# Kernel tuning notes

Measured on AMD Instinct MI355X. Metric: run time of the kernel, lower is better.

The kernel has to match this reference:

```python
import jax, jax.numpy as jnp
import numpy as np

B, LMAX, NCOND, NHID = 256, 512, 300, 600

def setup_inputs() -> dict:
    key = jax.random.key(0)
    ks = jax.random.split(key, 7)
    x = jax.random.normal(ks[0], (B, NCOND), dtype=jnp.float32)
    context = jax.random.normal(ks[1], (B, LMAX, NCOND), dtype=jnp.float32)
    lengths = jax.random.randint(ks[2], (B,), 0, LMAX, dtype=jnp.int32)
    W1 = jax.random.normal(ks[3], (NCOND, NHID), dtype=jnp.float32) * (1.0 / np.sqrt(NCOND))
    b1 = jax.random.normal(ks[4], (NHID,), dtype=jnp.float32) * 0.02
    Wa = jax.random.normal(ks[5], (NHID, NCOND), dtype=jnp.float32) * (1.0 / np.sqrt(NHID))
    ba = jax.random.normal(ks[6], (NCOND,), dtype=jnp.float32) * 0.02
    return {"x": x, "context": context, "lengths": lengths, "W1": W1, "b1": b1, "Wa": Wa, "ba": ba}

def reference(x, context, lengths, W1, b1, Wa, ba):
    # lengths clamped to >=1 (a ragged context is always non-empty)
    lens = jnp.maximum(lengths, 1)
    # valid-position mask over padded context: [B, L, 1]
    valid = (jnp.arange(LMAX)[None, :] < lens[:, None])[..., None].astype(context.dtype)
    # per-token MLP: relu(ctx @ W1 + b1)  -> [B, L, nhid]
    h = jax.nn.relu(jnp.einsum('blc,ch->blh', context, W1) + b1)
    # masked mean over valid tokens (ragged mean-pool) -> [B, nhid]
    pooled = jnp.sum(h * valid, axis=1) / lens[:, None].astype(context.dtype)
    # sigmoid gate -> [B, ncond], applied to x embeddings
    gate = jax.nn.sigmoid(jnp.einsum('bh,hc->bc', pooled, Wa) + ba)
    return gate * x
```

## Files before the change

### kernel.cpp

```cpp
#include <hip/hip_runtime.h>
#include <math.h>

#define BB     256
#define LMAX   512
#define NCOND  300
#define NHID   600
#define NSEG   8
#define CHUNK  64
#define KPAD   320
#define KLDS   328
#define NKC    10

#define AS1 __attribute__((address_space(1)))
#define AS3 __attribute__((address_space(3)))

typedef short s16x8 __attribute__((ext_vector_type(8)));
typedef float f32x4 __attribute__((ext_vector_type(4)));
typedef unsigned short u16x4 __attribute__((ext_vector_type(4)));

__device__ inline unsigned short f2bf(float f) {
    unsigned int x = __float_as_uint(f);
    x += 0x7fffu + ((x >> 16) & 1u);
    return (unsigned short)(x >> 16);
}

__global__ __launch_bounds__(256) void k0_w1t(const float* __restrict__ W1,
                                              unsigned short* __restrict__ w1t)
{
    const int t     = blockIdx.x * 256 + threadIdx.x;
    const int lane  = t & 63;
    const int g     = t >> 6;
    const int ntile = g / NKC;
    const int kc    = g - ntile * NKC;
    const int n     = ntile * 16 + (lane & 15);
    const int kbase = kc * 32 + (lane >> 4) * 8;
    union { unsigned short us[8]; s16x8 v8; } u;
#pragma unroll
    for (int j = 0; j < 8; ++j) {
        const int k = kbase + j;
        const float w = (n < NHID && k < NCOND) ? W1[(size_t)k * NHID + n] : 0.f;
        u.us[j] = f2bf(w);
    }
    *(s16x8*)(w1t + (size_t)t * 8) = u.v8;
}

__global__ __launch_bounds__(256) void k0b_cvt(const float* __restrict__ ctx,
                                               const int* __restrict__ lengths,
                                               unsigned short* __restrict__ ctx16)
{
    const int b = blockIdx.x, s = blockIdx.y, tid = threadIdx.x;
    int count = lengths[b]; if (count < 1) count = 1;
    if (s * CHUNK >= count) return;

    const size_t inbase  = ((size_t)b * LMAX + s * CHUNK) * NCOND;
    const float* src = ctx + inbase;
    char* dst = (char*)(ctx16 + ((size_t)b * LMAX + s * CHUNK) * KPAD);

#pragma unroll
    for (int i = 0; i < 20; ++i) {
        const int c   = i * 256 + tid;
        const int row = c / 80;
        const int q   = c - row * 80;
        float4 v = make_float4(0.f, 0.f, 0.f, 0.f);
        if (q < 75)
            v = *(const float4*)(src + (size_t)row * NCOND + q * 4);
        union { unsigned short us[4]; u16x4 v4; } o;
        o.us[0] = f2bf(v.x); o.us[1] = f2bf(v.y);
        o.us[2] = f2bf(v.z); o.us[3] = f2bf(v.w);
        const int off = (row * 640 + q * 8) ^ ((row & 7) << 4);
        *(u16x4*)(dst + off) = o.v4;
    }
}

__global__ __launch_bounds__(256, 3) void k1_mfma_dma(
    const unsigned short* __restrict__ ctx16, const int* __restrict__ lengths,
    const unsigned short* __restrict__ w1t, const float* __restrict__ b1,
    float* __restrict__ partial)
{
    const int b  = blockIdx.x;
    const int s  = blockIdx.y;
    const int ch = blockIdx.z;

    int count = lengths[b]; if (count < 1) count = 1;
    const int l0 = s * CHUNK;
    if (l0 >= count) return;
    const int valid = min(count - l0, CHUNK);

    const int tid  = threadIdx.x;
    const int lane = tid & 63;
    const int wv   = tid >> 6;
    const int ln15 = lane & 15;
    const int kg   = lane >> 4;

    __shared__ __align__(16) unsigned short atile[CHUNK * KPAD];

    const char* gsrc = (const char*)(ctx16 + ((size_t)b * LMAX + l0) * KPAD);
    char* lbase = (char*)atile;
#pragma unroll
    for (int r = 0; r < 10; ++r) {
        const int off = (r * 4 + wv) * 1024;
        __builtin_amdgcn_global_load_lds(
            (const AS1 void*)(gsrc + off + lane * 16),
            (AS3 void*)(lbase + off),
            16, 0, 0);
    }

    const int ntile0 = ch * 20 + wv * 5;
    const unsigned short* bbase = w1t + ((size_t)ntile0 * NKC * 64 + lane) * 8;
    s16x8 bf[2][5];
#pragma unroll
    for (int nt = 0; nt < 5; ++nt) bf[0][nt] = *(const s16x8*)(bbase + nt * 5120);

    __syncthreads();

    const int swz   = (ln15 & 7) << 4;
    const int abase = ln15 * 640 + kg * 16;
    const char* ab  = (const char*)atile;

    f32x4 acc[5][4];
#pragma unroll
    for (int nt = 0; nt < 5; ++nt)
#pragma unroll
        for (int mt = 0; mt < 4; ++mt) acc[nt][mt] = (f32x4){0.f, 0.f, 0.f, 0.f};

#pragma unroll
    for (int kc = 0; kc < NKC; ++kc) {
        const int cur = kc & 1, nxt = cur ^ 1;
        if (kc < NKC - 1) {
#pragma unroll
            for (int nt = 0; nt < 5; ++nt)
                bf[nxt][nt] = *(const s16x8*)(bbase + nt * 5120 + (kc + 1) * 512);
        }
        s16x8 af[4];
#pragma unroll
        for (int mt = 0; mt < 4; ++mt)
            af[mt] = *(const s16x8*)(ab + ((abase + mt * 10240 + kc * 64) ^ swz));
#pragma unroll
        for (int nt = 0; nt < 5; ++nt)
#pragma unroll
            for (int mt = 0; mt < 4; ++mt)
                acc[nt][mt] = __builtin_amdgcn_mfma_f32_16x16x32_bf16(
                    af[mt], bf[cur][nt], acc[nt][mt], 0, 0, 0);
    }

#pragma unroll
    for (int nt = 0; nt < 5; ++nt) {
        const int colg = ch * 320 + wv * 80 + nt * 16 + ln15;
        const float b1c = (colg < NHID) ? b1[colg] : 0.f;
        float ssum = 0.f;
#pragma unroll
        for (int mt = 0; mt < 4; ++mt) {
            const int rbase = mt * 16 + kg * 4;
#pragma unroll
            for (int r = 0; r < 4; ++r) {
                const float h = fmaxf(acc[nt][mt][r] + b1c, 0.f);
                if (rbase + r < valid) ssum += h;
            }
        }
        ssum += __shfl_xor(ssum, 16, 64);
        ssum += __shfl_xor(ssum, 32, 64);
        if (kg == 0 && colg < NHID)
            partial[((size_t)s * BB + b) * NHID + colg] = ssum;
    }
}

__global__ __launch_bounds__(256, 3) void k1_mfma_pool(
    const float* __restrict__ ctx, const int* __restrict__ lengths,
    const unsigned short* __restrict__ w1t, const float* __restrict__ b1,
    float* __restrict__ partial)
{
    const int b  = blockIdx.x;
    const int s  = blockIdx.y;
    const int ch = blockIdx.z;

    int count = lengths[b]; if (count < 1) count = 1;
    const int l0 = s * CHUNK;
    if (l0 >= count) return;
    const int valid = min(count - l0, CHUNK);

    const int tid  = threadIdx.x;
    const int lane = tid & 63;
    const int wv   = tid >> 6;
    const int ln15 = lane & 15;
    const int kg   = lane >> 4;

    __shared__ __align__(16) unsigned short atile[CHUNK * KLDS];

#pragma unroll
    for (int p = 0; p < 10; ++p) {
        const int i  = p * 256 + tid;
        const int r  = i / 40;
        const int c8 = i - r * 40;
        union { unsigned short us[8]; s16x8 v8; } u;
        if (r < valid && c8 < 38) {
            const float* src = ctx + ((size_t)b * LMAX + l0 + r) * NCOND + c8 * 8;
            const float4 v0 = *(const float4*)src;
            float4 v1 = make_float4(0.f, 0.f, 0.f, 0.f);
            if (c8 < 37) v1 = *(const float4*)(src + 4);
            u.us[0] = f2bf(v0.x); u.us[1] = f2bf(v0.y);
            u.us[2] = f2bf(v0.z); u.us[3] = f2bf(v0.w);
            u.us[4] = f2bf(v1.x); u.us[5] = f2bf(v1.y);
            u.us[6] = f2bf(v1.z); u.us[7] = f2bf(v1.w);
        } else {
#pragma unroll
            for (int j = 0; j < 8; ++j) u.us[j] = 0;
        }
        *(s16x8*)(atile + r * KLDS + c8 * 8) = u.v8;
    }
    __syncthreads();

    const int ntile0 = ch * 20 + wv * 5;
    const unsigned short* bbase = w1t + ((size_t)ntile0 * NKC * 64 + lane) * 8;
    const unsigned short* arow  = atile + ln15 * KLDS + kg * 8;

    f32x4 acc[5][4];
#pragma unroll
    for (int nt = 0; nt < 5; ++nt)
#pragma unroll
        for (int mt = 0; mt < 4; ++mt) acc[nt][mt] = (f32x4){0.f, 0.f, 0.f, 0.f};

    s16x8 bf[2][5];
#pragma unroll
    for (int nt = 0; nt < 5; ++nt) bf[0][nt] = *(const s16x8*)(bbase + nt * 5120);

#pragma unroll
    for (int kc = 0; kc < NKC; ++kc) {
        const int cur = kc & 1, nxt = cur ^ 1;
        if (kc < NKC - 1) {
#pragma unroll
            for (int nt = 0; nt < 5; ++nt)
                bf[nxt][nt] = *(const s16x8*)(bbase + nt * 5120 + (kc + 1) * 512);
        }
        s16x8 af[4];
#pragma unroll
        for (int mt = 0; mt < 4; ++mt)
            af[mt] = *(const s16x8*)(arow + mt * 16 * KLDS + kc * 32);
#pragma unroll
        for (int nt = 0; nt < 5; ++nt)
#pragma unroll
            for (int mt = 0; mt < 4; ++mt)
                acc[nt][mt] = __builtin_amdgcn_mfma_f32_16x16x32_bf16(
                    af[mt], bf[cur][nt], acc[nt][mt], 0, 0, 0);
    }

#pragma unroll
    for (int nt = 0; nt < 5; ++nt) {
        const int colg = ch * 320 + wv * 80 + nt * 16 + ln15;
        const float b1c = (colg < NHID) ? b1[colg] : 0.f;
        float ssum = 0.f;
#pragma unroll
        for (int mt = 0; mt < 4; ++mt) {
            const int rbase = mt * 16 + kg * 4;
#pragma unroll
            for (int r = 0; r < 4; ++r) {
                const float h = fmaxf(acc[nt][mt][r] + b1c, 0.f);
                if (rbase + r < valid) ssum += h;
            }
        }
        ssum += __shfl_xor(ssum, 16, 64);
        ssum += __shfl_xor(ssum, 32, 64);
        if (kg == 0 && colg < NHID)
            partial[((size_t)s * BB + b) * NHID + colg] = ssum;
    }
}

__global__ __launch_bounds__(640) void k2_gate(
    const float* __restrict__ x, const int* __restrict__ lengths,
    const float* __restrict__ partial, const float* __restrict__ Wa,
    const float* __restrict__ ba, float* __restrict__ out)
{
    const int b0  = blockIdx.x * 2;
    const int tid = threadIdx.x;

    __shared__ float pl[2][NHID];

    if (tid < NHID) {
#pragma unroll
        for (int bb = 0; bb < 2; ++bb) {
            int count = lengths[b0 + bb]; if (count < 1) count = 1;
            const int nch = (count + CHUNK - 1) >> 6;
            float ssum = 0.f;
            for (int sp = 0; sp < nch; ++sp)
                ssum += partial[((size_t)sp * BB + (b0 + bb)) * NHID + tid];
            pl[bb][tid] = ssum / (float)count;
        }
    }
    __syncthreads();

    if (tid < 2 * NCOND) {
        const int bb = tid / NCOND;
        const int n  = tid - bb * NCOND;
        const int b  = b0 + bb;
        float a0 = ba[n], a1 = 0.f, a2 = 0.f, a3 = 0.f;
        const float4* p4 = (const float4*)pl[bb];
        for (int h4 = 0; h4 < 148; h4 += 4) {
            const float4 pv0 = p4[h4];
            const float4 pv1 = p4[h4 + 1];
            const float4 pv2 = p4[h4 + 2];
            const float4 pv3 = p4[h4 + 3];
            const int hb = h4 * 4;
            a0 = fmaf(pv0.x, Wa[(size_t)(hb +  0) * NCOND + n], a0);
            a0 = fmaf(pv0.y, Wa[(size_t)(hb +  1) * NCOND + n], a0);
            a0 = fmaf(pv0.z, Wa[(size_t)(hb +  2) * NCOND + n], a0);
            a0 = fmaf(pv0.w, Wa[(size_t)(hb +  3) * NCOND + n], a0);
            a1 = fmaf(pv1.x, Wa[(size_t)(hb +  4) * NCOND + n], a1);
            a1 = fmaf(pv1.y, Wa[(size_t)(hb +  5) * NCOND + n], a1);
            a1 = fmaf(pv1.z, Wa[(size_t)(hb +  6) * NCOND + n], a1);
            a1 = fmaf(pv1.w, Wa[(size_t)(hb +  7) * NCOND + n], a1);
            a2 = fmaf(pv2.x, Wa[(size_t)(hb +  8) * NCOND + n], a2);
            a2 = fmaf(pv2.y, Wa[(size_t)(hb +  9) * NCOND + n], a2);
            a2 = fmaf(pv2.z, Wa[(size_t)(hb + 10) * NCOND + n], a2);
            a2 = fmaf(pv2.w, Wa[(size_t)(hb + 11) * NCOND + n], a2);
            a3 = fmaf(pv3.x, Wa[(size_t)(hb + 12) * NCOND + n], a3);
            a3 = fmaf(pv3.y, Wa[(size_t)(hb + 13) * NCOND + n], a3);
            a3 = fmaf(pv3.z, Wa[(size_t)(hb + 14) * NCOND + n], a3);
            a3 = fmaf(pv3.w, Wa[(size_t)(hb + 15) * NCOND + n], a3);
        }
        {
            const float4 pv0 = p4[148];
            const float4 pv1 = p4[149];
            a0 = fmaf(pv0.x, Wa[(size_t)592 * NCOND + n], a0);
            a0 = fmaf(pv0.y, Wa[(size_t)593 * NCOND + n], a0);
            a0 = fmaf(pv0.z, Wa[(size_t)594 * NCOND + n], a0);
            a0 = fmaf(pv0.w, Wa[(size_t)595 * NCOND + n], a0);
            a1 = fmaf(pv1.x, Wa[(size_t)596 * NCOND + n], a1);
            a1 = fmaf(pv1.y, Wa[(size_t)597 * NCOND + n], a1);
            a1 = fmaf(pv1.z, Wa[(size_t)598 * NCOND + n], a1);
            a1 = fmaf(pv1.w, Wa[(size_t)599 * NCOND + n], a1);
        }
        const float acc  = (a0 + a1) + (a2 + a3);
        const float gate = 1.0f / (1.0f + expf(-acc));
        out[(size_t)b * NCOND + n] = gate * x[(size_t)b * NCOND + n];
    }
}

extern "C" void kernel_launch(void* const* d_in, const int* in_sizes, int n_in,
                              void* d_out, int out_size, void* d_ws, size_t ws_size,
                              hipStream_t stream)
{
    const float* x       = (const float*)d_in[0];
    const float* ctx     = (const float*)d_in[1];
    const int*   lengths = (const int*)  d_in[2];
    const float* W1      = (const float*)d_in[3];
    const float* b1      = (const float*)d_in[4];
    const float* Wa      = (const float*)d_in[5];
    const float* ba      = (const float*)d_in[6];
    float*       out     = (float*)d_out;

    const size_t W1T_B   = 409600;
    const size_t PART_B  = 4915200;
    const size_t CTX16_B = (size_t)BB * LMAX * KPAD * 2;
    const size_t NEED    = W1T_B + PART_B + CTX16_B;

    unsigned short* w1t     = (unsigned short*)d_ws;
    float*          partial = (float*)((char*)d_ws + W1T_B);

    k0_w1t<<<100, 256, 0, stream>>>(W1, w1t);

    if (ws_size >= NEED) {
        unsigned short* ctx16 = (unsigned short*)((char*)d_ws + W1T_B + PART_B);
        k0b_cvt<<<dim3(BB, NSEG), 256, 0, stream>>>(ctx, lengths, ctx16);
        k1_mfma_dma<<<dim3(BB, NSEG, 2), 256, 0, stream>>>(ctx16, lengths, w1t, b1, partial);
    } else {
        k1_mfma_pool<<<dim3(BB, NSEG, 2), 256, 0, stream>>>(ctx, lengths, w1t, b1, partial);
    }

    k2_gate<<<BB / 2, 640, 0, stream>>>(x, lengths, partial, Wa, ba, out);
}
```

Measured before the change: 309.5 us.

## Split GEMM M dimension across 8 waves and widen bf16 conversion stores

The main MFMA kernel now uses 512 threads per block. Two wave halves each compute half of the 64 token rows, so each wave holds 10 accumulators instead of 20, and the halves' row sums are reduced through shared memory before the write. A-fragment LDS reads are double-buffered alongside the B loads. The conversion kernel now processes 8 floats per thread and issues 16-byte stores. The aim is more waves in flight and lower register pressure, at the cost of loading the B fragments twice per block and adding an extra barrier and reduction.

```diff
diff --git a/kernel.cpp b/kernel.cpp
--- a/kernel.cpp
+++ b/kernel.cpp
@@ -16,7 +16,7 @@
 
 typedef short s16x8 __attribute__((ext_vector_type(8)));
 typedef float f32x4 __attribute__((ext_vector_type(4)));
-typedef unsigned short u16x4 __attribute__((ext_vector_type(4)));
+typedef unsigned short u16x8 __attribute__((ext_vector_type(8)));
 
 __device__ inline unsigned short f2bf(float f) {
     unsigned int x = __float_as_uint(f);
@@ -52,27 +52,30 @@
     int count = lengths[b]; if (count < 1) count = 1;
     if (s * CHUNK >= count) return;
 
-    const size_t inbase  = ((size_t)b * LMAX + s * CHUNK) * NCOND;
-    const float* src = ctx + inbase;
+    const float* src = ctx + ((size_t)b * LMAX + s * CHUNK) * NCOND;
     char* dst = (char*)(ctx16 + ((size_t)b * LMAX + s * CHUNK) * KPAD);
 
 #pragma unroll
-    for (int i = 0; i < 20; ++i) {
+    for (int i = 0; i < 10; ++i) {
         const int c   = i * 256 + tid;
-        const int row = c / 80;
-        const int q   = c - row * 80;
-        float4 v = make_float4(0.f, 0.f, 0.f, 0.f);
-        if (q < 75)
-            v = *(const float4*)(src + (size_t)row * NCOND + q * 4);
-        union { unsigned short us[4]; u16x4 v4; } o;
-        o.us[0] = f2bf(v.x); o.us[1] = f2bf(v.y);
-        o.us[2] = f2bf(v.z); o.us[3] = f2bf(v.w);
-        const int off = (row * 640 + q * 8) ^ ((row & 7) << 4);
-        *(u16x4*)(dst + off) = o.v4;
-    }
-}
-
-__global__ __launch_bounds__(256, 3) void k1_mfma_dma(
+        const int row = c / 40;
+        const int q2  = c - row * 40;
+        float4 v0 = make_float4(0.f, 0.f, 0.f, 0.f);
+        float4 v1 = make_float4(0.f, 0.f, 0.f, 0.f);
+        const float* rsrc = src + (size_t)row * NCOND + q2 * 8;
+        if (q2 < 38) v0 = *(const float4*)rsrc;
+        if (q2 < 37) v1 = *(const float4*)(rsrc + 4);
+        union { unsigned short us[8]; u16x8 v8; } o;
+        o.us[0] = f2bf(v0.x); o.us[1] = f2bf(v0.y);
+        o.us[2] = f2bf(v0.z); o.us[3] = f2bf(v0.w);
+        o.us[4] = f2bf(v1.x); o.us[5] = f2bf(v1.y);
+        o.us[6] = f2bf(v1.z); o.us[7] = f2bf(v1.w);
+        const int off = (row * 640 + q2 * 16) ^ ((row & 7) << 4);
+        *(u16x8*)(dst + off) = o.v8;
+    }
+}
+
+__global__ __launch_bounds__(512, 4) void k1_dma2(
     const unsigned short* __restrict__ ctx16, const int* __restrict__ lengths,
     const unsigned short* __restrict__ w1t, const float* __restrict__ b1,
     float* __restrict__ partial)
@@ -89,178 +92,99 @@
     const int tid  = threadIdx.x;
     const int lane = tid & 63;
     const int wv   = tid >> 6;
+    const int wvn  = wv & 3;
+    const int mh   = wv >> 2;
     const int ln15 = lane & 15;
     const int kg   = lane >> 4;
 
     __shared__ __align__(16) unsigned short atile[CHUNK * KPAD];
+    __shared__ float red[320];
 
     const char* gsrc = (const char*)(ctx16 + ((size_t)b * LMAX + l0) * KPAD);
     char* lbase = (char*)atile;
 #pragma unroll
-    for (int r = 0; r < 10; ++r) {
-        const int off = (r * 4 + wv) * 1024;
+    for (int i = 0; i < 5; ++i) {
+        const int off = (i * 8 + wv) * 1024;
         __builtin_amdgcn_global_load_lds(
             (const AS1 void*)(gsrc + off + lane * 16),
-            (AS3 void*)(lbase + off),
-            16, 0, 0);
-    }
-
-    const int ntile0 = ch * 20 + wv * 5;
-    const unsigned short* bbase = w1t + ((size_t)ntile0 * NKC * 64 + lane) * 8;
+            (AS3 void*)(lbase + off), 16, 0, 0);
+    }
+
+    const unsigned short* bbase = w1t + ((size_t)(ch * 20 + wvn * 5) * NKC * 64 + lane) * 8;
     s16x8 bf[2][5];
 #pragma unroll
     for (int nt = 0; nt < 5; ++nt) bf[0][nt] = *(const s16x8*)(bbase + nt * 5120);
 
+    const int swz    = (ln15 & 7) << 4;
+    const int abyte0 = ln15 * 640 + kg * 16 + (mh * 2) * 10240;
+    const char* ab   = (const char*)atile;
+
+    f32x4 acc[5][2];
+#pragma unroll
+    for (int nt = 0; nt < 5; ++nt) {
+        acc[nt][0] = (f32x4){0.f, 0.f, 0.f, 0.f};
+        acc[nt][1] = (f32x4){0.f, 0.f, 0.f, 0.f};
+    }
+
     __syncthreads();
 
-    const int swz   = (ln15 & 7) << 4;
-    const int abase = ln15 * 640 + kg * 16;
-    const char* ab  = (const char*)atile;
-
-    f32x4 acc[5][4];
-#pragma unroll
-    for (int nt = 0; nt < 5; ++nt)
-#pragma unroll
-        for (int mt = 0; mt < 4; ++mt) acc[nt][mt] = (f32x4){0.f, 0.f, 0.f, 0.f};
+    s16x8 af[2][2];
+    af[0][0] = *(const s16x8*)(ab + ((abyte0)         ^ swz));
+    af[0][1] = *(const s16x8*)(ab + ((abyte0 + 10240) ^ swz));
 
 #pragma unroll
     for (int kc = 0; kc < NKC; ++kc) {
         const int cur = kc & 1, nxt = cur ^ 1;
         if (kc < NKC - 1) {
+            af[nxt][0] = *(const s16x8*)(ab + ((abyte0 +         (kc + 1) * 64) ^ swz));
+            af[nxt][1] = *(const s16x8*)(ab + ((abyte0 + 10240 + (kc + 1) * 64) ^ swz));
 #pragma unroll
             for (int nt = 0; nt < 5; ++nt)
                 bf[nxt][nt] = *(const s16x8*)(bbase + nt * 5120 + (kc + 1) * 512);
         }
-        s16x8 af[4];
-#pragma unroll
-        for (int mt = 0; mt < 4; ++mt)
-            af[mt] = *(const s16x8*)(ab + ((abase + mt * 10240 + kc * 64) ^ swz));
-#pragma unroll
-        for (int nt = 0; nt < 5; ++nt)
-#pragma unroll
-            for (int mt = 0; mt < 4; ++mt)
-                acc[nt][mt] = __builtin_amdgcn_mfma_f32_16x16x32_bf16(
-                    af[mt], bf[cur][nt], acc[nt][mt], 0, 0, 0);
-    }
-
+#pragma unroll
+        for (int nt = 0; nt < 5; ++nt) {
+            acc[nt][0] = __builtin_amdgcn_mfma_f32_16x16x32_bf16(
+                af[cur][0], bf[cur][nt], acc[nt][0], 0, 0, 0);
+            acc[nt][1] = __builtin_amdgcn_mfma_f32_16x16x32_bf16(
+                af[cur][1], bf[cur][nt], acc[nt][1], 0, 0, 0);
+        }
+    }
+
+    float sfin[5];
 #pragma unroll
     for (int nt = 0; nt < 5; ++nt) {
-        const int colg = ch * 320 + wv * 80 + nt * 16 + ln15;
+        const int colg = ch * 320 + wvn * 80 + nt * 16 + ln15;
         const float b1c = (colg < NHID) ? b1[colg] : 0.f;
         float ssum = 0.f;
 #pragma unroll
-        for (int mt = 0; mt < 4; ++mt) {
-            const int rbase = mt * 16 + kg * 4;
+        for (int j = 0; j < 2; ++j) {
+            const int rbase = (mh * 2 + j) * 16 + kg * 4;
 #pragma unroll
             for (int r = 0; r < 4; ++r) {
-                const float h = fmaxf(acc[nt][mt][r] + b1c, 0.f);
+                const float h = fmaxf(acc[nt][j][r] + b1c, 0.f);
                 if (rbase + r < valid) ssum += h;
             }
         }
         ssum += __shfl_xor(ssum, 16, 64);
         ssum += __shfl_xor(ssum, 32, 64);
-        if (kg == 0 && colg < NHID)
-            partial[((size_t)s * BB + b) * NHID + colg] = ssum;
-    }
-}
-
-__global__ __launch_bounds__(256, 3) void k1_mfma_pool(
-    const float* __restrict__ ctx, const int* __restrict__ lengths,
-    const unsigned short* __restrict__ w1t, const float* __restrict__ b1,
-    float* __restrict__ partial)
-{
-    const int b  = blockIdx.x;
-    const int s  = blockIdx.y;
-    const int ch = blockIdx.z;
-
-    int count = lengths[b]; if (count < 1) count = 1;
-    const int l0 = s * CHUNK;
-    if (l0 >= count) return;
-    const int valid = min(count - l0, CHUNK);
-
-    const int tid  = threadIdx.x;
-    const int lane = tid & 63;
-    const int wv   = tid >> 6;
-    const int ln15 = lane & 15;
-    const int kg   = lane >> 4;
-
-    __shared__ __align__(16) unsigned short atile[CHUNK * KLDS];
-
-#pragma unroll
-    for (int p = 0; p < 10; ++p) {
-        const int i  = p * 256 + tid;
-        const int r  = i / 40;
-        const int c8 = i - r * 40;
-        union { unsigned short us[8]; s16x8 v8; } u;
-        if (r < valid && c8 < 38) {
-            const float* src = ctx + ((size_t)b * LMAX + l0 + r) * NCOND + c8 * 8;
-            const float4 v0 = *(const float4*)src;
-            float4 v1 = make_float4(0.f, 0.f, 0.f, 0.f);
-            if (c8 < 37) v1 = *(const float4*)(src + 4);
-            u.us[0] = f2bf(v0.x); u.us[1] = f2bf(v0.y);
-            u.us[2] = f2bf(v0.z); u.us[3] = f2bf(v0.w);
-            u.us[4] = f2bf(v1.x); u.us[5] = f2bf(v1.y);
-            u.us[6] = f2bf(v1.z); u.us[7] = f2bf(v1.w);
-        } else {
-#pragma unroll
-            for (int j = 0; j < 8; ++j) u.us[j] = 0;
-        }
-        *(s16x8*)(atile + r * KLDS + c8 * 8) = u.v8;
+        sfin[nt] = ssum;
+    }
+
+    if (mh == 1) {
+#pragma unroll
+        for (int nt = 0; nt < 5; ++nt)
+            if (kg == 0) red[wvn * 80 + nt * 16 + ln15] = sfin[nt];
     }
     __syncthreads();
-
-    const int ntile0 = ch * 20 + wv * 5;
-    const unsigned short* bbase = w1t + ((size_t)ntile0 * NKC * 64 + lane) * 8;
-    const unsigned short* arow  = atile + ln15 * KLDS + kg * 8;
-
-    f32x4 acc[5][4];
-#pragma unroll
-    for (int nt = 0; nt < 5; ++nt)
-#pragma unroll
-        for (int mt = 0; mt < 4; ++mt) acc[nt][mt] = (f32x4){0.f, 0.f, 0.f, 0.f};
-
-    s16x8 bf[2][5];
-#pragma unroll
-    for (int nt = 0; nt < 5; ++nt) bf[0][nt] = *(const s16x8*)(bbase + nt * 5120);
-
-#pragma unroll
-    for (int kc = 0; kc < NKC; ++kc) {
-        const int cur = kc & 1, nxt = cur ^ 1;
-        if (kc < NKC - 1) {
-#pragma unroll
-            for (int nt = 0; nt < 5; ++nt)
-                bf[nxt][nt] = *(const s16x8*)(bbase + nt * 5120 + (kc + 1) * 512);
-        }
-        s16x8 af[4];
-#pragma unroll
-        for (int mt = 0; mt < 4; ++mt)
-            af[mt] = *(const s16x8*)(arow + mt * 16 * KLDS + kc * 32);
-#pragma unroll
-        for (int nt = 0; nt < 5; ++nt)
-#pragma unroll
-            for (int mt = 0; mt < 4; ++mt)
-                acc[nt][mt] = __builtin_amdgcn_mfma_f32_16x16x32_bf16(
-                    af[mt], bf[cur][nt], acc[nt][mt], 0, 0, 0);
-    }
-
-#pragma unroll
-    for (int nt = 0; nt < 5; ++nt) {
-        const int colg = ch * 320 + wv * 80 + nt * 16 + ln15;
-        const float b1c = (colg < NHID) ? b1[colg] : 0.f;
-        float ssum = 0.f;
-#pragma unroll
-        for (int mt = 0; mt < 4; ++mt) {
-            const int rbase = mt * 16 + kg * 4;
-#pragma unroll
-            for (int r = 0; r < 4; ++r) {
-                const float h = fmaxf(acc[nt][mt][r] + b1c, 0.f);
-                if (rbase + r < valid) ssum += h;
-            }
-        }
-        ssum += __shfl_xor(ssum, 16, 64);
-        ssum += __shfl_xor(ssum, 32, 64);
-        if (kg == 0 && colg < NHID)
-            partial[((size_t)s * BB + b) * NHID + colg] = ssum;
+    if (mh == 0) {
+#pragma unroll
+        for (int nt = 0; nt < 5; ++nt) {
+            const int colg = ch * 320 + wvn * 80 + nt * 16 + ln15;
+            const float v = sfin[nt] + red[wvn * 80 + nt * 16 + ln15];
+            if (kg == 0 && colg < NHID)
+                partial[((size_t)s * BB + b) * NHID + colg] = v;
+        }
     }
 }
 
@@ -334,6 +258,106 @@
     }
 }
 
+__global__ __launch_bounds__(256, 3) void k1_mfma_pool(
+    const float* __restrict__ ctx, const int* __restrict__ lengths,
+    const unsigned short* __restrict__ w1t, const float* __restrict__ b1,
+    float* __restrict__ partial)
+{
+    const int b  = blockIdx.x;
+    const int s  = blockIdx.y;
+    const int ch = blockIdx.z;
+
+    int count = lengths[b]; if (count < 1) count = 1;
+    const int l0 = s * CHUNK;
+    if (l0 >= count) return;
+    const int valid = min(count - l0, CHUNK);
+
+    const int tid  = threadIdx.x;
+    const int lane = tid & 63;
+    const int wv   = tid >> 6;
+    const int ln15 = lane & 15;
+    const int kg   = lane >> 4;
+
+    __shared__ __align__(16) unsigned short atile[CHUNK * KLDS];
+
+#pragma unroll
+    for (int p = 0; p < 10; ++p) {
+        const int i  = p * 256 + tid;
+        const int r  = i / 40;
+        const int c8 = i - r * 40;
+        union { unsigned short us[8]; s16x8 v8; } u;
+        if (r < valid && c8 < 38) {
+            const float* src = ctx + ((size_t)b * LMAX + l0 + r) * NCOND + c8 * 8;
+            const float4 v0 = *(const float4*)src;
+            float4 v1 = make_float4(0.f, 0.f, 0.f, 0.f);
+            if (c8 < 37) v1 = *(const float4*)(src + 4);
+            u.us[0] = f2bf(v0.x); u.us[1] = f2bf(v0.y);
+            u.us[2] = f2bf(v0.z); u.us[3] = f2bf(v0.w);
+            u.us[4] = f2bf(v1.x); u.us[5] = f2bf(v1.y);
+            u.us[6] = f2bf(v1.z); u.us[7] = f2bf(v1.w);
+        } else {
+#pragma unroll
+            for (int j = 0; j < 8; ++j) u.us[j] = 0;
+        }
+        *(s16x8*)(atile + r * KLDS + c8 * 8) = u.v8;
+    }
+    __syncthreads();
+
+    const int ntile0 = ch * 20 + wv * 5;
+    const unsigned short* bbase = w1t + ((size_t)ntile0 * NKC * 64 + lane) * 8;
+    const unsigned short* arow  = atile + ln15 * KLDS + kg * 8;
+
+    f32x4 acc[5][4];
+#pragma unroll
+    for (int nt = 0; nt < 5; ++nt)
+#pragma unroll
+        for (int mt = 0; mt < 4; ++mt) acc[nt][mt] = (f32x4){0.f, 0.f, 0.f, 0.f};
+
+    s16x8 bf[2][5];
+#pragma unroll
+    for (int nt = 0; nt < 5; ++nt) bf[0][nt] = *(const s16x8*)(bbase + nt * 5120);
+
+#pragma unroll
+    for (int kc = 0; kc < NKC; ++kc) {
+        const int cur = kc & 1, nxt = cur ^ 1;
+        if (kc < NKC - 1) {
+#pragma unroll
+            for (int nt = 0; nt < 5; ++nt)
+                bf[nxt][nt] = *(const s16x8*)(bbase + nt * 5120 + (kc + 1) * 512);
+        }
+        s16x8 af[4];
+#pragma unroll
+        for (int mt = 0; mt < 4; ++mt)
+            af[mt] = *(const s16x8*)(arow + mt * 16 * KLDS + kc * 32);
+#pragma unroll
+        for (int nt = 0; nt < 5; ++nt)
+#pragma unroll
+            for (int mt = 0; mt < 4; ++mt)
+                acc[nt][mt] = __builtin_amdgcn_mfma_f32_16x16x32_bf16(
+                    af[mt], bf[cur][nt], acc[nt][mt], 0, 0, 0);
+    }
+
+#pragma unroll
+    for (int nt = 0; nt < 5; ++nt) {
+        const int colg = ch * 320 + wv * 80 + nt * 16 + ln15;
+        const float b1c = (colg < NHID) ? b1[colg] : 0.f;
+        float ssum = 0.f;
+#pragma unroll
+        for (int mt = 0; mt < 4; ++mt) {
+            const int rbase = mt * 16 + kg * 4;
+#pragma unroll
+            for (int r = 0; r < 4; ++r) {
+                const float h = fmaxf(acc[nt][mt][r] + b1c, 0.f);
+                if (rbase + r < valid) ssum += h;
+            }
+        }
+        ssum += __shfl_xor(ssum, 16, 64);
+        ssum += __shfl_xor(ssum, 32, 64);
+        if (kg == 0 && colg < NHID)
+            partial[((size_t)s * BB + b) * NHID + colg] = ssum;
+    }
+}
+
 extern "C" void kernel_launch(void* const* d_in, const int* in_sizes, int n_in,
                               void* d_out, int out_size, void* d_ws, size_t ws_size,
                               hipStream_t stream)
@@ -360,7 +384,7 @@
     if (ws_size >= NEED) {
         unsigned short* ctx16 = (unsigned short*)((char*)d_ws + W1T_B + PART_B);
         k0b_cvt<<<dim3(BB, NSEG), 256, 0, stream>>>(ctx, lengths, ctx16);
-        k1_mfma_dma<<<dim3(BB, NSEG, 2), 256, 0, stream>>>(ctx16, lengths, w1t, b1, partial);
+        k1_dma2<<<dim3(BB, NSEG, 2), 512, 0, stream>>>(ctx16, lengths, w1t, b1, partial);
     } else {
         k1_mfma_pool<<<dim3(BB, NSEG, 2), 256, 0, stream>>>(ctx, lengths, w1t, b1, partial);
     }
```

Result: slower. 323.8 us (+4.6%).
